# Optimization experiments

Hardware: AMD Instinct MI355X
Metric: run time of the kernel (lower is better)

Reference implementation:

```python
import jax, jax.numpy as jnp
import numpy as np

N_NODES = 100000
N_EDGES = 1600000
VOCAB = 2048
NODE_DIM = 64
HIDDEN = 64
N_MASK = 10000


def setup_inputs() -> dict:
    key = jax.random.key(0)
    ks = jax.random.split(key, 10)
    x = jax.random.randint(ks[0], (N_NODES, 1), 0, VOCAB, dtype=jnp.int64)
    edge_index = jax.random.randint(ks[1], (2, N_EDGES), 0, N_NODES, dtype=jnp.int64)
    mask_x_position = jax.random.randint(ks[2], (N_MASK,), 0, N_NODES, dtype=jnp.int64)
    # embedding init: normal with std = node_dim ** -0.5 (as in initialize_parameters)
    emb = jax.random.normal(ks[3], (VOCAB, NODE_DIM), dtype=jnp.float32) * (NODE_DIM ** -0.5)
    # SAGEConv layer 1: lin_l (neighbors, with bias), lin_r (root, no bias)
    s1 = (NODE_DIM ** -0.5)
    W_l1 = jax.random.uniform(ks[4], (NODE_DIM, HIDDEN), jnp.float32, -s1, s1)
    b_l1 = jnp.zeros((HIDDEN,), jnp.float32)
    W_r1 = jax.random.uniform(ks[5], (NODE_DIM, HIDDEN), jnp.float32, -s1, s1)
    # SAGEConv layer 2
    s2 = (HIDDEN ** -0.5)
    W_l2 = jax.random.uniform(ks[6], (HIDDEN, VOCAB), jnp.float32, -s2, s2)
    b_l2 = jnp.zeros((VOCAB,), jnp.float32)
    W_r2 = jax.random.uniform(ks[7], (HIDDEN, VOCAB), jnp.float32, -s2, s2)
    return {"x": x, "edge_index": edge_index, "mask_x_position": mask_x_position,
            "emb": emb, "W_l1": W_l1, "b_l1": b_l1, "W_r1": W_r1,
            "W_l2": W_l2, "b_l2": b_l2, "W_r2": W_r2}


def _sage_conv(h, src, dst, W_l, b_l, W_r):
    # mean-aggregate source-node features at destination nodes (PyG SAGEConv, aggr='mean')
    msgs = h[src]                                                  # [E, D]
    agg = jax.ops.segment_sum(msgs, dst, num_segments=N_NODES)     # [N, D]
    deg = jax.ops.segment_sum(jnp.ones((src.shape[0], 1), h.dtype), dst,
                              num_segments=N_NODES)                # [N, 1]
    mean = agg / jnp.maximum(deg, 1.0)
    return mean @ W_l + b_l + h @ W_r


def reference(x, edge_index, mask_x_position, emb, W_l1, b_l1, W_r1, W_l2, b_l2, W_r2):
    src, dst = edge_index[0], edge_index[1]
    h = emb[x[:, 0]]                                # embedding(x).squeeze(1) -> [N, node_dim]
    # dropout is identity in eval mode
    h = _sage_conv(h, src, dst, W_l1, b_l1, W_r1)   # [N, hidden]
    h = jax.nn.relu(h)
    h = _sage_conv(h, src, dst, W_l2, b_l2, W_r2)   # [N, vocab]
    return jax.nn.log_softmax(h[mask_x_position], axis=1)
```

## Files before the change

### kernel.cpp

```cpp
#include <hip/hip_runtime.h>
#include <math.h>

#define N_NODES   100000
#define N_EDGES   1600000
#define VOCAB     2048
#define NODE_DIM  64
#define HIDDEN    64
#define N_MASK    10000

#define BN        96
#define NBKT      1042
#define CHUNK     2048
#define NCH       782
#define ELCAP     2048

typedef __attribute__((ext_vector_type(8))) short short8;
typedef __attribute__((ext_vector_type(4))) float f32x4;
typedef unsigned short ushort_t;
typedef unsigned int uint_t;

#define H1_OFF      0
#define ESRC_OFF    25600000
#define E2_OFF      32000000
#define EWL_OFF     44800000
#define EWR_OFF     45324288
#define W2T_OFF     45848576
#define X2B_OFF     46372864
#define ROWPTR_OFF  48932864
#define BCNT_OFF    49332880
#define BPTR_OFF    49337056
#define MAT_OFF     49341232

__device__ __forceinline__ ushort_t f2bf(float f) {
    uint_t u = __builtin_bit_cast(uint_t, f);
    u += 0x7FFFu + ((u >> 16) & 1u);
    return (ushort_t)(u >> 16);
}

__global__ __launch_bounds__(256) void k_prep(const float* __restrict__ emb,
                                              const float* __restrict__ Wl1,
                                              const float* __restrict__ Wr1,
                                              const float* __restrict__ Wl2,
                                              const float* __restrict__ Wr2,
                                              float* __restrict__ embWl,
                                              float* __restrict__ embWr,
                                              ushort_t* __restrict__ W2T) {
    __shared__ ushort_t T[64 * 66];
    const int bx = blockIdx.x;
    const int tid = threadIdx.x;
    if (bx < 1024) {
        const int half = bx >> 9;
        const float* W = half ? Wr1 : Wl1;
        float* out = half ? embWr : embWl;
        int idx = (bx & 511) * 256 + tid;
        int v = idx >> 6, c = idx & 63;
        float s = 0.0f;
#pragma unroll 8
        for (int k = 0; k < 64; k++) s += emb[v * 64 + k] * W[k * 64 + c];
        out[idx] = s;
    } else {
        int t = bx - 1024;
        const int k0 = (t & 1) * 64;
        const int n0 = (t >> 1) * 64;
        const float* Wsrc = (k0 == 0) ? Wl2 : Wr2;
#pragma unroll
        for (int i = 0; i < 16; i++) {
            int idx = i * 256 + tid;
            int k = idx >> 6, n = idx & 63;
            T[n * 66 + k] = f2bf(Wsrc[(size_t)k * VOCAB + n0 + n]);
        }
        __syncthreads();
#pragma unroll
        for (int i = 0; i < 16; i++) {
            int idx = i * 256 + tid;
            int n = idx >> 6, k = idx & 63;
            W2T[(size_t)(n0 + n) * 128 + k0 + k] = T[n * 66 + k];
        }
    }
}

__global__ __launch_bounds__(256) void k_count2(const int* __restrict__ dst,
                                                ushort_t* __restrict__ mat) {
    __shared__ int hist[NBKT];
    const int c = blockIdx.x, t = threadIdx.x;
    const int e0 = c * CHUNK;
    const int n = min(CHUNK, N_EDGES - e0);
    for (int i = t; i < NBKT; i += 256) hist[i] = 0;
    int d[8];
#pragma unroll
    for (int i = 0; i < 8; i++) {
        int idx = i * 256 + t;
        d[i] = (idx < n) ? dst[e0 + idx] : -1;
    }
    __syncthreads();
#pragma unroll
    for (int i = 0; i < 8; i++)
        if (d[i] >= 0) atomicAdd(&hist[d[i] / BN], 1);
    __syncthreads();
    for (int i = t; i < NBKT; i += 256) mat[(size_t)c * NBKT + i] = (ushort_t)hist[i];
}

__global__ __launch_bounds__(1024) void k_mscan(ushort_t* __restrict__ mat,
                                                int* __restrict__ bcnt) {
    __shared__ int s[1024];
    const int b = blockIdx.x, t = threadIdx.x;
    int v = (t < NCH) ? (int)mat[(size_t)t * NBKT + b] : 0;
    s[t] = v;
    __syncthreads();
    for (int off = 1; off < 1024; off <<= 1) {
        int a = (t >= off) ? s[t - off] : 0;
        __syncthreads();
        s[t] += a;
        __syncthreads();
    }
    if (t < NCH) mat[(size_t)t * NBKT + b] = (ushort_t)(s[t] - v);
    if (t == NCH - 1) bcnt[b] = s[t];
}

__global__ __launch_bounds__(1024) void k_bscan(const int* __restrict__ bcnt,
                                                int* __restrict__ bptr,
                                                int* __restrict__ rowptr) {
    __shared__ int s[1024];
    int t = threadIdx.x;
    int i0 = 2 * t, i1 = 2 * t + 1;
    int a = (i0 < NBKT) ? bcnt[i0] : 0;
    int b = (i1 < NBKT) ? bcnt[i1] : 0;
    int v = a + b;
    s[t] = v;
    __syncthreads();
    for (int off = 1; off < 1024; off <<= 1) {
        int p = (t >= off) ? s[t - off] : 0;
        __syncthreads();
        s[t] += p;
        __syncthreads();
    }
    int excl = s[t] - v;
    if (i0 < NBKT) bptr[i0] = excl;
    if (i1 < NBKT) bptr[i1] = excl + a;
    if (t == 1023) bptr[NBKT] = s[t];
    if (t == 0) rowptr[N_NODES] = N_EDGES;
}

__global__ __launch_bounds__(256) void k_scatter3(const int* __restrict__ src,
                                                  const int* __restrict__ dst,
                                                  const int* __restrict__ x,
                                                  const ushort_t* __restrict__ mat,
                                                  const int* __restrict__ bptr,
                                                  int2* __restrict__ e2) {
    __shared__ int cur[NBKT];
    const int c = blockIdx.x, t = threadIdx.x;
    const int e0 = c * CHUNK;
    const int n = min(CHUNK, N_EDGES - e0);
    for (int i = t; i < NBKT; i += 256)
        cur[i] = bptr[i] + (int)mat[(size_t)c * NBKT + i];
    int d[8], sv[8], voc[8];
#pragma unroll
    for (int i = 0; i < 8; i++) {
        int idx = i * 256 + t;
        if (idx < n) { d[i] = dst[e0 + idx]; sv[i] = src[e0 + idx]; }
        else d[i] = -1;
    }
#pragma unroll
    for (int i = 0; i < 8; i++)
        if (d[i] >= 0) voc[i] = x[sv[i]];
    __syncthreads();
#pragma unroll
    for (int i = 0; i < 8; i++) {
        if (d[i] >= 0) {
            int b = d[i] / BN;
            int pos = atomicAdd(&cur[b], 1);
            e2[pos] = make_int2(sv[i], (voc[i] << 8) | (d[i] - b * BN));
        }
    }
}

__global__ __launch_bounds__(512) void k_sortagg(const int* __restrict__ bptr,
                                                 const int2* __restrict__ e2,
                                                 const int* __restrict__ x,
                                                 const float* __restrict__ embWl,
                                                 const float* __restrict__ embWr,
                                                 const float* __restrict__ b1,
                                                 int* __restrict__ rowptr,
                                                 int* __restrict__ esrc,
                                                 float* __restrict__ h1) {
    __shared__ int2 eL[ELCAP];
    __shared__ int sc[128];
    __shared__ int cur[BN];
    __shared__ int base[BN + 1];
    const int b = blockIdx.x;
    const int t = threadIdx.x;
    const int r0 = bptr[b], r1 = bptr[b + 1];
    const int m = r1 - r0;

    int2 ev[4];
#pragma unroll
    for (int k = 0; k < 4; k++) {
        int i = r0 + t + k * 512;
        ev[k] = (i < r1) ? e2[i] : make_int2(-1, 0);
    }
    if (t < 128) sc[t] = 0;
    __syncthreads();

#pragma unroll
    for (int k = 0; k < 4; k++)
        if (ev[k].x >= 0) atomicAdd(&sc[ev[k].y & 255], 1);
    __syncthreads();
    int v = (t < 128) ? sc[t] : 0;
    for (int off = 1; off < 128; off <<= 1) {
        int a = (t >= off && t < 128) ? sc[t - off] : 0;
        __syncthreads();
        if (t < 128) sc[t] += a;
        __syncthreads();
    }
    if (t < BN) {
        int excl = sc[t] - v;
        base[t] = excl;
        cur[t] = excl;
        int node = b * BN + t;
        if (node < N_NODES) rowptr[node] = r0 + excl;
        if (t == BN - 1) base[BN] = sc[t];
    }
    __syncthreads();
#pragma unroll
    for (int k = 0; k < 4; k++) {
        if (ev[k].x >= 0) {
            int pos = atomicAdd(&cur[ev[k].y & 255], 1);
            eL[pos] = ev[k];
        }
    }
    __syncthreads();
    for (int i = t; i < m; i += 512)
        esrc[r0 + i] = eL[i].x;

    const int wv = t >> 6, lane = t & 63;
    const float b1v = b1[lane];
    for (int nl = wv; nl < BN; nl += 8) {
        int node = b * BN + nl;
        if (node >= N_NODES) break;
        int j0 = base[nl], j1 = base[nl + 1];
        int deg = j1 - j0;
        float s0 = 0.f, s1 = 0.f, s2 = 0.f, s3 = 0.f;
        float s4 = 0.f, s5 = 0.f, s6 = 0.f, s7 = 0.f;
        int j = j0;
        for (; j + 7 < j1; j += 8) {
            int y0 = eL[j].y,     y1 = eL[j + 1].y, y2 = eL[j + 2].y, y3 = eL[j + 3].y;
            int y4 = eL[j + 4].y, y5 = eL[j + 5].y, y6 = eL[j + 6].y, y7 = eL[j + 7].y;
            s0 += embWl[((y0 >> 8) << 6) + lane];
            s1 += embWl[((y1 >> 8) << 6) + lane];
            s2 += embWl[((y2 >> 8) << 6) + lane];
            s3 += embWl[((y3 >> 8) << 6) + lane];
            s4 += embWl[((y4 >> 8) << 6) + lane];
            s5 += embWl[((y5 >> 8) << 6) + lane];
            s6 += embWl[((y6 >> 8) << 6) + lane];
            s7 += embWl[((y7 >> 8) << 6) + lane];
        }
        for (; j + 3 < j1; j += 4) {
            int y0 = eL[j].y, y1 = eL[j + 1].y, y2 = eL[j + 2].y, y3 = eL[j + 3].y;
            s0 += embWl[((y0 >> 8) << 6) + lane];
            s1 += embWl[((y1 >> 8) << 6) + lane];
            s2 += embWl[((y2 >> 8) << 6) + lane];
            s3 += embWl[((y3 >> 8) << 6) + lane];
        }
        for (; j < j1; j++)
            s0 += embWl[((eL[j].y >> 8) << 6) + lane];
        float sum = ((s0 + s1) + (s2 + s3)) + ((s4 + s5) + (s6 + s7));
        float inv = 1.0f / fmaxf((float)deg, 1.0f);
        float self = embWr[(x[node] << 6) + lane];
        h1[((size_t)node << 6) + lane] = fmaxf(sum * inv + self + b1v, 0.0f);
    }
}

__global__ __launch_bounds__(256) void k_x2(const int* __restrict__ mask,
                                            const int* __restrict__ rowptr,
                                            const int* __restrict__ esrc,
                                            const float* __restrict__ h1,
                                            ushort_t* __restrict__ X2b) {
    int gw = (blockIdx.x * 256 + threadIdx.x) >> 6;
    int lane = threadIdx.x & 63;
    if (gw >= N_MASK) return;
    int n = mask[gw];
    int r0 = rowptr[n], r1 = rowptr[n + 1];
    int deg = r1 - r0;
    float s0 = 0.f, s1 = 0.f, s2 = 0.f, s3 = 0.f;
    float s4 = 0.f, s5 = 0.f, s6 = 0.f, s7 = 0.f;
    for (int base = 0; base < deg; base += 64) {
        int cnt = min(64, deg - base);
        int mys = (base + lane < deg) ? esrc[r0 + base + lane] : 0;
        int t = 0;
        for (; t + 7 < cnt; t += 8) {
            int sa = __shfl(mys, t),     sb = __shfl(mys, t + 1);
            int sc = __shfl(mys, t + 2), sd = __shfl(mys, t + 3);
            int se = __shfl(mys, t + 4), sf = __shfl(mys, t + 5);
            int sg = __shfl(mys, t + 6), sh = __shfl(mys, t + 7);
            s0 += h1[((size_t)sa << 6) + lane];
            s1 += h1[((size_t)sb << 6) + lane];
            s2 += h1[((size_t)sc << 6) + lane];
            s3 += h1[((size_t)sd << 6) + lane];
            s4 += h1[((size_t)se << 6) + lane];
            s5 += h1[((size_t)sf << 6) + lane];
            s6 += h1[((size_t)sg << 6) + lane];
            s7 += h1[((size_t)sh << 6) + lane];
        }
        for (; t + 3 < cnt; t += 4) {
            int sa = __shfl(mys, t),     sb = __shfl(mys, t + 1);
            int sc = __shfl(mys, t + 2), sd = __shfl(mys, t + 3);
            s0 += h1[((size_t)sa << 6) + lane];
            s1 += h1[((size_t)sb << 6) + lane];
            s2 += h1[((size_t)sc << 6) + lane];
            s3 += h1[((size_t)sd << 6) + lane];
        }
        for (; t < cnt; t++)
            s0 += h1[((size_t)__shfl(mys, t) << 6) + lane];
    }
    float sum = ((s0 + s1) + (s2 + s3)) + ((s4 + s5) + (s6 + s7));
    float inv = 1.0f / fmaxf((float)deg, 1.0f);
    X2b[gw * 128 + lane]      = f2bf(sum * inv);
    X2b[gw * 128 + 64 + lane] = f2bf(h1[((size_t)n << 6) + lane]);
}

__global__ __launch_bounds__(256) void k_gemm2_mfma(const ushort_t* __restrict__ X2b,
                                                    const ushort_t* __restrict__ W2T,
                                                    const float* __restrict__ bias,
                                                    float* __restrict__ out,
                                                    int M) {
    __shared__ ushort_t As[64 * 144];
    __shared__ ushort_t Bs[64 * 144];
    const int tid  = threadIdx.x;
    const int row0 = blockIdx.x * 64;
    const int col0 = blockIdx.y * 64;

#pragma unroll
    for (int i = 0; i < 4; i++) {
        int idx = i * 256 + tid;
        int r = idx >> 4, ch = idx & 15;
        int R = row0 + r;
        short8 v = {0, 0, 0, 0, 0, 0, 0, 0};
        if (R < M) v = *(const short8*)(X2b + (size_t)R * 128 + ch * 8);
        *(short8*)(As + r * 144 + ch * 8) = v;
    }
#pragma unroll
    for (int i = 0; i < 4; i++) {
        int idx = i * 256 + tid;
        int r = idx >> 4, ch = idx & 15;
        *(short8*)(Bs + r * 144 + ch * 8) =
            *(const short8*)(W2T + (size_t)(col0 + r) * 128 + ch * 8);
    }
    __syncthreads();

    const int lane = tid & 63;
    const int wv   = tid >> 6;
    const int wr = wv >> 1, wc = wv & 1;
    const int l15 = lane & 15, q = lane >> 4;

    f32x4 acc[2][2] = {};
    const ushort_t* Abase = As + (wr * 32 + l15) * 144 + q * 8;
    const ushort_t* Bbase = Bs + (wc * 32 + l15) * 144 + q * 8;

#pragma unroll
    for (int ks = 0; ks < 4; ks++) {
        short8 a0 = *(const short8*)(Abase + ks * 32);
        short8 a1 = *(const short8*)(Abase + 16 * 144 + ks * 32);
        short8 b0 = *(const short8*)(Bbase + ks * 32);
        short8 b1 = *(const short8*)(Bbase + 16 * 144 + ks * 32);
        acc[0][0] = __builtin_amdgcn_mfma_f32_16x16x32_bf16(a0, b0, acc[0][0], 0, 0, 0);
        acc[0][1] = __builtin_amdgcn_mfma_f32_16x16x32_bf16(a0, b1, acc[0][1], 0, 0, 0);
        acc[1][0] = __builtin_amdgcn_mfma_f32_16x16x32_bf16(a1, b0, acc[1][0], 0, 0, 0);
        acc[1][1] = __builtin_amdgcn_mfma_f32_16x16x32_bf16(a1, b1, acc[1][1], 0, 0, 0);
    }

#pragma unroll
    for (int ni = 0; ni < 2; ni++) {
        int c_ = col0 + wc * 32 + ni * 16 + l15;
        float bv = bias[c_];
#pragma unroll
        for (int mi = 0; mi < 2; mi++) {
#pragma unroll
            for (int reg = 0; reg < 4; reg++) {
                int r_ = row0 + wr * 32 + mi * 16 + q * 4 + reg;
                if (r_ < M) out[(size_t)r_ * VOCAB + c_] = acc[mi][ni][reg] + bv;
            }
        }
    }
}

__global__ __launch_bounds__(256) void k_logsoftmax(float* __restrict__ out) {
    const int row = blockIdx.x;
    float4* p4 = (float4*)(out + (size_t)row * VOCAB);
    const int tid = threadIdx.x;
    float4 v[2];
    float m = -INFINITY;
#pragma unroll
    for (int i = 0; i < 2; i++) {
        v[i] = p4[tid + i * 256];
        m = fmaxf(m, fmaxf(fmaxf(v[i].x, v[i].y), fmaxf(v[i].z, v[i].w)));
    }
#pragma unroll
    for (int off = 1; off < 64; off <<= 1) m = fmaxf(m, __shfl_xor(m, off));
    __shared__ float redm[4];
    __shared__ float reds[4];
    int wave = tid >> 6;
    if ((tid & 63) == 0) redm[wave] = m;
    __syncthreads();
    m = fmaxf(fmaxf(redm[0], redm[1]), fmaxf(redm[2], redm[3]));
    float s = 0.0f;
#pragma unroll
    for (int i = 0; i < 2; i++)
        s += expf(v[i].x - m) + expf(v[i].y - m) + expf(v[i].z - m) + expf(v[i].w - m);
#pragma unroll
    for (int off = 1; off < 64; off <<= 1) s += __shfl_xor(s, off);
    if ((tid & 63) == 0) reds[wave] = s;
    __syncthreads();
    s = reds[0] + reds[1] + reds[2] + reds[3];
    float L = m + logf(s);
#pragma unroll
    for (int i = 0; i < 2; i++) {
        float4 o = v[i];
        o.x -= L; o.y -= L; o.z -= L; o.w -= L;
        p4[tid + i * 256] = o;
    }
}

extern "C" void kernel_launch(void* const* d_in, const int* in_sizes, int n_in,
                              void* d_out, int out_size, void* d_ws, size_t ws_size,
                              hipStream_t stream) {
    const int*   x    = (const int*)d_in[0];
    const int*   ei   = (const int*)d_in[1];
    const int*   src  = ei;
    const int*   dst  = ei + N_EDGES;
    const int*   mask = (const int*)d_in[2];
    const float* emb  = (const float*)d_in[3];
    const float* Wl1  = (const float*)d_in[4];
    const float* bl1  = (const float*)d_in[5];
    const float* Wr1  = (const float*)d_in[6];
    const float* Wl2  = (const float*)d_in[7];
    const float* bl2  = (const float*)d_in[8];
    const float* Wr2  = (const float*)d_in[9];
    float* out = (float*)d_out;

    char* ws = (char*)d_ws;
    float*    h1     = (float*)(ws + H1_OFF);
    int*      esrc   = (int*)(ws + ESRC_OFF);
    int2*     e2     = (int2*)(ws + E2_OFF);
    float*    embWl  = (float*)(ws + EWL_OFF);
    float*    embWr  = (float*)(ws + EWR_OFF);
    ushort_t* W2T    = (ushort_t*)(ws + W2T_OFF);
    ushort_t* X2b    = (ushort_t*)(ws + X2B_OFF);
    int*      rowptr = (int*)(ws + ROWPTR_OFF);
    int*      bcnt   = (int*)(ws + BCNT_OFF);
    int*      bptr   = (int*)(ws + BPTR_OFF);
    ushort_t* mat    = (ushort_t*)(ws + MAT_OFF);

    k_count2  <<<NCH, 256, 0, stream>>>(dst, mat);
    k_mscan   <<<NBKT, 1024, 0, stream>>>(mat, bcnt);
    k_bscan   <<<1, 1024, 0, stream>>>(bcnt, bptr, rowptr);
    k_scatter3<<<NCH, 256, 0, stream>>>(src, dst, x, mat, bptr, e2);

    k_prep<<<1088, 256, 0, stream>>>(emb, Wl1, Wr1, Wl2, Wr2, embWl, embWr, W2T);

    k_sortagg<<<NBKT, 512, 0, stream>>>(bptr, e2, x, embWl, embWr, bl1, rowptr, esrc, h1);

    k_x2<<<(N_MASK * 64 + 255) / 256, 256, 0, stream>>>(mask, rowptr, esrc, h1, X2b);
    dim3 g2((N_MASK + 63) / 64, VOCAB / 64);
    k_gemm2_mfma<<<g2, 256, 0, stream>>>(X2b, W2T, bl2, out, N_MASK);

    k_logsoftmax<<<N_MASK, 256, 0, stream>>>(out);
}
```

Before: 259.8 us.

## Fuse second-layer GEMM with log-softmax in one row-block kernel

Replaces the tiled MFMA GEMM and the separate log-softmax kernel with a single kernel. Each block computes 16 full output rows across all 2048 columns, with 8 waves each covering 256 columns, and keeps the accumulators in registers. Row max and sum are reduced through shuffles and shared memory before the final log-probabilities are written. This removes the write and re-read of the 10000x2048 logits and one launch. In exchange, B operands are read directly from global memory without shared tiling, and register pressure rises to 64 accumulator floats per lane.

```diff
diff --git a/kernel.cpp b/kernel.cpp
--- a/kernel.cpp
+++ b/kernel.cpp
@@ -318,105 +318,105 @@
     X2b[gw * 128 + 64 + lane] = f2bf(h1[((size_t)n << 6) + lane]);
 }
 
-__global__ __launch_bounds__(256) void k_gemm2_mfma(const ushort_t* __restrict__ X2b,
-                                                    const ushort_t* __restrict__ W2T,
-                                                    const float* __restrict__ bias,
-                                                    float* __restrict__ out,
-                                                    int M) {
-    __shared__ ushort_t As[64 * 144];
-    __shared__ ushort_t Bs[64 * 144];
-    const int tid  = threadIdx.x;
-    const int row0 = blockIdx.x * 64;
-    const int col0 = blockIdx.y * 64;
-
-#pragma unroll
-    for (int i = 0; i < 4; i++) {
-        int idx = i * 256 + tid;
-        int r = idx >> 4, ch = idx & 15;
-        int R = row0 + r;
-        short8 v = {0, 0, 0, 0, 0, 0, 0, 0};
-        if (R < M) v = *(const short8*)(X2b + (size_t)R * 128 + ch * 8);
-        *(short8*)(As + r * 144 + ch * 8) = v;
-    }
-#pragma unroll
-    for (int i = 0; i < 4; i++) {
-        int idx = i * 256 + tid;
-        int r = idx >> 4, ch = idx & 15;
-        *(short8*)(Bs + r * 144 + ch * 8) =
-            *(const short8*)(W2T + (size_t)(col0 + r) * 128 + ch * 8);
-    }
-    __syncthreads();
-
-    const int lane = tid & 63;
-    const int wv   = tid >> 6;
-    const int wr = wv >> 1, wc = wv & 1;
+__global__ __launch_bounds__(512) void k_gemm2_ls(const ushort_t* __restrict__ X2b,
+                                                  const ushort_t* __restrict__ W2T,
+                                                  const float* __restrict__ bias,
+                                                  float* __restrict__ out) {
+    __shared__ ushort_t As[16 * 144];
+    __shared__ float redm[16][8];
+    __shared__ float reds[16][8];
+    const int tid = threadIdx.x;
+    const int row0 = blockIdx.x * 16;
+
+    if (tid < 256) {
+        int r = tid >> 4, ch = tid & 15;
+        *(short8*)(As + r * 144 + ch * 8) =
+            *(const short8*)(X2b + (size_t)(row0 + r) * 128 + ch * 8);
+    }
+    __syncthreads();
+
+    const int lane = tid & 63, wv = tid >> 6;
     const int l15 = lane & 15, q = lane >> 4;
-
-    f32x4 acc[2][2] = {};
-    const ushort_t* Abase = As + (wr * 32 + l15) * 144 + q * 8;
-    const ushort_t* Bbase = Bs + (wc * 32 + l15) * 144 + q * 8;
-
-#pragma unroll
-    for (int ks = 0; ks < 4; ks++) {
-        short8 a0 = *(const short8*)(Abase + ks * 32);
-        short8 a1 = *(const short8*)(Abase + 16 * 144 + ks * 32);
-        short8 b0 = *(const short8*)(Bbase + ks * 32);
-        short8 b1 = *(const short8*)(Bbase + 16 * 144 + ks * 32);
-        acc[0][0] = __builtin_amdgcn_mfma_f32_16x16x32_bf16(a0, b0, acc[0][0], 0, 0, 0);
-        acc[0][1] = __builtin_amdgcn_mfma_f32_16x16x32_bf16(a0, b1, acc[0][1], 0, 0, 0);
-        acc[1][0] = __builtin_amdgcn_mfma_f32_16x16x32_bf16(a1, b0, acc[1][0], 0, 0, 0);
-        acc[1][1] = __builtin_amdgcn_mfma_f32_16x16x32_bf16(a1, b1, acc[1][1], 0, 0, 0);
-    }
-
-#pragma unroll
-    for (int ni = 0; ni < 2; ni++) {
-        int c_ = col0 + wc * 32 + ni * 16 + l15;
-        float bv = bias[c_];
-#pragma unroll
-        for (int mi = 0; mi < 2; mi++) {
-#pragma unroll
-            for (int reg = 0; reg < 4; reg++) {
-                int r_ = row0 + wr * 32 + mi * 16 + q * 4 + reg;
-                if (r_ < M) out[(size_t)r_ * VOCAB + c_] = acc[mi][ni][reg] + bv;
-            }
-        }
-    }
-}
-
-__global__ __launch_bounds__(256) void k_logsoftmax(float* __restrict__ out) {
-    const int row = blockIdx.x;
-    float4* p4 = (float4*)(out + (size_t)row * VOCAB);
-    const int tid = threadIdx.x;
-    float4 v[2];
-    float m = -INFINITY;
-#pragma unroll
-    for (int i = 0; i < 2; i++) {
-        v[i] = p4[tid + i * 256];
-        m = fmaxf(m, fmaxf(fmaxf(v[i].x, v[i].y), fmaxf(v[i].z, v[i].w)));
-    }
-#pragma unroll
-    for (int off = 1; off < 64; off <<= 1) m = fmaxf(m, __shfl_xor(m, off));
-    __shared__ float redm[4];
-    __shared__ float reds[4];
-    int wave = tid >> 6;
-    if ((tid & 63) == 0) redm[wave] = m;
-    __syncthreads();
-    m = fmaxf(fmaxf(redm[0], redm[1]), fmaxf(redm[2], redm[3]));
-    float s = 0.0f;
-#pragma unroll
-    for (int i = 0; i < 2; i++)
-        s += expf(v[i].x - m) + expf(v[i].y - m) + expf(v[i].z - m) + expf(v[i].w - m);
-#pragma unroll
-    for (int off = 1; off < 64; off <<= 1) s += __shfl_xor(s, off);
-    if ((tid & 63) == 0) reds[wave] = s;
-    __syncthreads();
-    s = reds[0] + reds[1] + reds[2] + reds[3];
-    float L = m + logf(s);
-#pragma unroll
-    for (int i = 0; i < 2; i++) {
-        float4 o = v[i];
-        o.x -= L; o.y -= L; o.z -= L; o.w -= L;
-        p4[tid + i * 256] = o;
+    const int col0 = wv * 256;
+
+    short8 a[4];
+#pragma unroll
+    for (int ks = 0; ks < 4; ks++)
+        a[ks] = *(const short8*)(As + l15 * 144 + q * 8 + ks * 32);
+
+    f32x4 acc[16] = {};
+#pragma unroll
+    for (int ct = 0; ct < 16; ct++) {
+        const ushort_t* Bb = W2T + (size_t)(col0 + ct * 16 + l15) * 128 + q * 8;
+        short8 b0 = *(const short8*)(Bb);
+        short8 b1 = *(const short8*)(Bb + 32);
+        short8 b2 = *(const short8*)(Bb + 64);
+        short8 b3 = *(const short8*)(Bb + 96);
+        acc[ct] = __builtin_amdgcn_mfma_f32_16x16x32_bf16(a[0], b0, acc[ct], 0, 0, 0);
+        acc[ct] = __builtin_amdgcn_mfma_f32_16x16x32_bf16(a[1], b1, acc[ct], 0, 0, 0);
+        acc[ct] = __builtin_amdgcn_mfma_f32_16x16x32_bf16(a[2], b2, acc[ct], 0, 0, 0);
+        acc[ct] = __builtin_amdgcn_mfma_f32_16x16x32_bf16(a[3], b3, acc[ct], 0, 0, 0);
+    }
+
+    float mx[4] = {-INFINITY, -INFINITY, -INFINITY, -INFINITY};
+#pragma unroll
+    for (int ct = 0; ct < 16; ct++) {
+        float bv = bias[col0 + ct * 16 + l15];
+#pragma unroll
+        for (int r = 0; r < 4; r++) {
+            acc[ct][r] += bv;
+            mx[r] = fmaxf(mx[r], acc[ct][r]);
+        }
+    }
+#pragma unroll
+    for (int off = 1; off < 16; off <<= 1)
+#pragma unroll
+        for (int r = 0; r < 4; r++)
+            mx[r] = fmaxf(mx[r], __shfl_xor(mx[r], off));
+    if (l15 == 0)
+#pragma unroll
+        for (int r = 0; r < 4; r++) redm[q * 4 + r][wv] = mx[r];
+    __syncthreads();
+#pragma unroll
+    for (int r = 0; r < 4; r++) {
+        float m_ = redm[q * 4 + r][0];
+#pragma unroll
+        for (int w = 1; w < 8; w++) m_ = fmaxf(m_, redm[q * 4 + r][w]);
+        mx[r] = m_;
+    }
+
+    float sm[4] = {0.f, 0.f, 0.f, 0.f};
+#pragma unroll
+    for (int ct = 0; ct < 16; ct++)
+#pragma unroll
+        for (int r = 0; r < 4; r++)
+            sm[r] += expf(acc[ct][r] - mx[r]);
+#pragma unroll
+    for (int off = 1; off < 16; off <<= 1)
+#pragma unroll
+        for (int r = 0; r < 4; r++)
+            sm[r] += __shfl_xor(sm[r], off);
+    if (l15 == 0)
+#pragma unroll
+        for (int r = 0; r < 4; r++) reds[q * 4 + r][wv] = sm[r];
+    __syncthreads();
+    float L[4];
+#pragma unroll
+    for (int r = 0; r < 4; r++) {
+        float s_ = reds[q * 4 + r][0];
+#pragma unroll
+        for (int w = 1; w < 8; w++) s_ += reds[q * 4 + r][w];
+        L[r] = mx[r] + logf(s_);
+    }
+
+#pragma unroll
+    for (int ct = 0; ct < 16; ct++) {
+        int c_ = col0 + ct * 16 + l15;
+#pragma unroll
+        for (int r = 0; r < 4; r++) {
+            int r_ = row0 + q * 4 + r;
+            out[(size_t)r_ * VOCAB + c_] = acc[ct][r] - L[r];
+        }
     }
 }
 
@@ -460,8 +460,5 @@
     k_sortagg<<<NBKT, 512, 0, stream>>>(bptr, e2, x, embWl, embWr, bl1, rowptr, esrc, h1);
 
     k_x2<<<(N_MASK * 64 + 255) / 256, 256, 0, stream>>>(mask, rowptr, esrc, h1, X2b);
-    dim3 g2((N_MASK + 63) / 64, VOCAB / 64);
-    k_gemm2_mfma<<<g2, 256, 0, stream>>>(X2b, W2T, bl2, out, N_MASK);
-
-    k_logsoftmax<<<N_MASK, 256, 0, stream>>>(out);
-}
+    k_gemm2_ls<<<N_MASK / 16, 512, 0, stream>>>(X2b, W2T, bl2, out);
+}
```

New measurement: 273.5 us. 5.3% more time.
